# Kernel tuning notes

Hardware: AMD Instinct MI355X
Metric: run time of the kernel (lower is better)

## Reference

```python
import jax, jax.numpy as jnp
import numpy as np
import math

K = 20; M = 10; N = K * M; DEG = N - 1; AJR = 30; HID = 96
NH = 4; HD = HID + 2 + K; DM = NH * HD  # 472


def _graph():
    # complete graph: node i receives edges from all j != i (fixed in-degree DEG)
    idx = jnp.arange(N)
    j = jnp.arange(DEG)
    srcs = jnp.where(j[None, :] < idx[:, None], j[None, :], j[None, :] + 1)  # [N, DEG]
    grp = idx // M
    same = (grp[srcs] == grp[:, None]).astype(jnp.float32)  # e_type[:,1]
    return srcs, same


def _pe_table(max_step, dim):
    pos = np.arange(max_step)[:, None].astype(np.float32)
    div = np.exp(np.arange(0, dim, 2).astype(np.float32) * -(math.log(10000.0) / dim))
    pe = np.zeros((max_step, dim), np.float32)
    pe[:, 0::2] = np.sin(pos * div)
    pe[:, 1::2] = np.cos(pos * div)
    return jnp.asarray(pe)


def _gcn(h, x, label, w, d, srcs, same, p):
    (l0w, l0b, l1w, l1b, l2w, l2b, l3w, l3b, l4w, l4b, l5w, l5b) = p
    t0 = 1.0 - same
    h_src = h[srcs]                      # [N, DEG, HID] gather
    we = w[..., None]
    n1_v = (h_src * we * t0[..., None]).sum(1) / (w * t0).sum(1, keepdims=True)
    n2_v = (h_src * we * same[..., None]).sum(1) / (w * same).sum(1, keepdims=True)
    n1_e = jnp.sort(d * t0, axis=1)[:, ::-1][:, :AJR]      # top-AJR cross-group dists
    n2_e = jnp.sort(d * same, axis=1)[:, ::-1][:, :M - 1]  # top-(m-1) same-group dists
    return jax.nn.relu(x @ l0w + l0b + label @ l1w + l1b + n1_v @ l2w + l2b
                       + n2_v @ l3w + l3b + n1_e @ l4w + l4b + n2_e @ l5w + l5b)


def _forward(x, label, h0, w, d,
             l0_w, l0_b, l1_w, l1_b, l2_w, l2_b, l3_w, l3_b, l4_w, l4_b, l5_w, l5_b,
             mha_w0, mha_b0, mha_w1, mha_b1, mha_w3, mha_b3,
             v1_w, v1_b, v2_w, v2_b, gnn_step, max_step, remain_step):
    srcs, same = _graph()
    gcn_p = (l0_w, l0_b, l1_w, l1_b, l2_w, l2_b, l3_w, l3_b, l4_w, l4_b, l5_w, l5_b)
    h = h0
    for _ in range(gnn_step):
        h = _gcn(h, x, label, w, d, srcs, same, gcn_p)
    pe = _pe_table(max_step, HID)
    h_full = jnp.concatenate([h + pe[remain_step], x, label], axis=1)  # [N, HD]
    gc = h_full.T @ label / M                                          # [HD, K]
    kv = jnp.tile(h_full, (1, NH))                                     # [N, DM]
    kh = (kv @ mha_w0 + mha_b0).reshape(N, NH, HD).transpose(1, 0, 2)  # keys use linears[0]
    vh = (kv @ mha_w1 + mha_b1).reshape(N, NH, HD).transpose(1, 0, 2)  # values use linears[1]
    h_rep = jnp.repeat(h_full, N, axis=0)      # torch repeat(1,n).view(n*n, hd)
    h_tile = jnp.tile(h_full, (N, 1))          # torch repeat(n,1)
    la_rep = jnp.repeat(label, N, axis=0) @ gc.T
    la_tile = jnp.tile(label, (N, 1)) @ gc.T
    Q1 = jnp.concatenate([h_rep, h_tile, la_rep, la_tile], axis=1)  # [N*N, DM]
    Q2 = jnp.concatenate([h_tile, h_rep, la_tile, la_rep], axis=1)
    inv_sqrt_dk = 1.0 / jnp.sqrt(jnp.float32(HD))

    def attend(Q):
        q = (Q @ mha_w0 + mha_b0).reshape(-1, NH, HD)
        s = jnp.einsum('bhd,hkd->bhk', q, kh) * inv_sqrt_dk
        p = jax.nn.softmax(s, axis=-1)
        o = jnp.einsum('bhk,hkd->bhd', p, vh).reshape(-1, DM)
        return o @ mha_w3 + mha_b3

    S = attend(Q1) + attend(Q2)               # [N*N, DM]
    S_a_encoding = S[:, None, :]              # [N*N, 1, DM]
    Q_sa = (jax.nn.relu(S @ v1_w + v1_b) @ v2_w + v2_b).squeeze()  # [N*N]
    return S_a_encoding, h, h_full, Q_sa


def setup_inputs() -> dict:
    key = jax.random.key(0)
    ks = jax.random.split(key, 32)
    def rn(i, shape, s=1.0):
        return jax.random.normal(ks[i], shape, jnp.float32) * s
    grp = jnp.arange(N) // M
    label = jax.nn.one_hot(grp, K, dtype=jnp.float32)
    return {
        'x': rn(0, (N, 2)),
        'label': label,
        'h0': rn(1, (N, HID)),
        'w': jax.random.uniform(ks[2], (N, DEG), jnp.float32, 0.1, 1.0),
        'd': jax.random.uniform(ks[3], (N, DEG), jnp.float32, 0.0, 1.0),
        'l0_w': rn(4, (2, HID), 0.5), 'l0_b': rn(5, (HID,), 0.05),
        'l1_w': rn(6, (K, HID), 0.2), 'l1_b': rn(7, (HID,), 0.05),
        'l2_w': rn(8, (HID, HID), 0.1), 'l2_b': rn(9, (HID,), 0.05),
        'l3_w': rn(10, (HID, HID), 0.1), 'l3_b': rn(11, (HID,), 0.05),
        'l4_w': rn(12, (AJR, HID), 0.15), 'l4_b': rn(13, (HID,), 0.05),
        'l5_w': rn(14, (M - 1, HID), 0.3), 'l5_b': rn(15, (HID,), 0.05),
        'mha_w0': rn(16, (DM, DM), 0.04), 'mha_b0': rn(17, (DM,), 0.02),
        'mha_w1': rn(18, (DM, DM), 0.04), 'mha_b1': rn(19, (DM,), 0.02),
        'mha_w3': rn(20, (DM, DM), 0.04), 'mha_b3': rn(21, (DM,), 0.02),
        'v1_w': rn(22, (DM, HID // 2), 0.04), 'v1_b': rn(23, (HID // 2,), 0.02),
        'v2_w': rn(24, (HID // 2, 1), 0.1), 'v2_b': rn(25, (1,), 0.02),
        'gnn_step': 2, 'max_step': 50, 'remain_step': 10,
    }


def reference(x, label, h0, w, d,
              l0_w, l0_b, l1_w, l1_b, l2_w, l2_b, l3_w, l3_b, l4_w, l4_b, l5_w, l5_b,
              mha_w0, mha_b0, mha_w1, mha_b1, mha_w3, mha_b3,
              v1_w, v1_b, v2_w, v2_b, gnn_step, max_step, remain_step):
    return _forward(x, label, h0, w, d,
                    l0_w, l0_b, l1_w, l1_b, l2_w, l2_b, l3_w, l3_b, l4_w, l4_b, l5_w, l5_b,
                    mha_w0, mha_b0, mha_w1, mha_b1, mha_w3, mha_b3,
                    v1_w, v1_b, v2_w, v2_b, gnn_step, max_step, remain_step)
```

## Files before the change

kernel.cpp:

```cpp
#include <hip/hip_runtime.h>
#include <hip/hip_bf16.h>
#include <math.h>

typedef unsigned short ushort;
typedef unsigned int uint;

#define NV 200
#define DEG 199
#define HID 96
#define KG 20
#define MG 10
#define AJR 30
#define NH 4
#define HD 118
#define DM 472
#define NN 40000
#define NT 20100
#define NTP 20160

#define WS_BASE   0
#define WS_H1     19200
#define WS_H2     38400
#define WS_HFULL  57600
#define WS_KHF    194952
#define WS_VHF    289352
#define WS_B1     383752
#define WS_B2     478152
#define WS_SC1    572552
#define WS_SC2    732552
#define WS_ZT     1315464

#define OFF_H   18880000
#define OFF_HF  18899200
#define OFF_Q   18922800

typedef __attribute__((ext_vector_type(8))) short short8v;
typedef __attribute__((ext_vector_type(4))) float float4v;

__device__ __forceinline__ ushort f2bf(float f) {
  uint u = __float_as_uint(f);
  uint r = (u + 0x7fffu + ((u >> 16) & 1u)) >> 16;
  return (ushort)r;
}
__device__ __forceinline__ uint packbf(float a, float b) {
  __hip_bfloat162 h2 = __float22bfloat162_rn(make_float2(a, b));
  union { __hip_bfloat162 h; uint u; } c;
  c.h = h2;
  return c.u;
}

__device__ __forceinline__ int triOff(int i) {
  return i * 200 - ((i * (i - 1)) >> 1);
}
__device__ __forceinline__ void p2ij(int p, int& io, int& jo) {
  float s = sqrtf((float)(160801 - 8 * p));
  int i = (int)((401.0f - s) * 0.5f);
  if (i < 0) i = 0;
  if (i > 199) i = 199;
  while (i > 0 && triOff(i) > p) --i;
  while (i < 199 && triOff(i + 1) <= p) ++i;
  io = i;
  jo = i + (p - triOff(i));
}

__global__ __launch_bounds__(256) void k_base(
    const float* __restrict__ x, const float* __restrict__ dmat,
    const float* __restrict__ label,
    const float* __restrict__ l0w, const float* __restrict__ l0b,
    const float* __restrict__ l1w, const float* __restrict__ l1b,
    const float* __restrict__ l2b, const float* __restrict__ l3b,
    const float* __restrict__ l4w, const float* __restrict__ l4b,
    const float* __restrict__ l5w, const float* __restrict__ l5b,
    float* __restrict__ base) {
  int i = blockIdx.x; int t = threadIdx.x;
  int g = i / MG;
  __shared__ float sv[256];
  __shared__ float sn2[9];
  float v = -1.0f;
  if (t < DEG) {
    int u = (t < i) ? t : t + 1;
    if (u / MG != g) v = dmat[i * DEG + t];
  }
  sv[t] = v;
  __syncthreads();
  for (int k2 = 2; k2 <= 256; k2 <<= 1) {
    for (int jj = k2 >> 1; jj > 0; jj >>= 1) {
      int ixj = t ^ jj;
      if (ixj > t) {
        float a = sv[t], b = sv[ixj];
        bool sw = ((t & k2) == 0) ? (a < b) : (a > b);
        if (sw) { sv[t] = b; sv[ixj] = a; }
      }
      __syncthreads();
    }
  }
  if (t == 0) {
    float tmp[9];
    for (int q = 0; q < 9; q++) tmp[q] = dmat[i * DEG + MG * g + q];
    for (int a2 = 1; a2 < 9; a2++) {
      float key = tmp[a2]; int b2 = a2 - 1;
      while (b2 >= 0 && tmp[b2] < key) { tmp[b2 + 1] = tmp[b2]; b2--; }
      tmp[b2 + 1] = key;
    }
    for (int q = 0; q < 9; q++) sn2[q] = tmp[q];
  }
  __syncthreads();
  if (t < HID) {
    float acc = l0b[t] + l1b[t] + l2b[t] + l3b[t] + l4b[t] + l5b[t];
    acc += x[i * 2 + 0] * l0w[t] + x[i * 2 + 1] * l0w[HID + t];
    for (int k = 0; k < KG; k++) acc += label[i * KG + k] * l1w[k * HID + t];
    for (int q = 0; q < AJR; q++) acc += sv[q] * l4w[q * HID + t];
    for (int q = 0; q < 9; q++) acc += sn2[q] * l5w[q * HID + t];
    base[i * HID + t] = acc;
  }
}

__global__ __launch_bounds__(512) void k_gcn4(
    const float* __restrict__ hin, const float* __restrict__ base,
    const float* __restrict__ w, const float* __restrict__ l2w,
    const float* __restrict__ l3w, float* __restrict__ hout) {
  int i = blockIdx.x; int t = threadIdx.x;
  int g = i / MG;
  __shared__ float pJ[4][HID], wJ[4][HID];
  __shared__ float n1s[HID], n2s[HID];
  __shared__ float m[4][HID];
  if (t < 384) {
    int q = t / HID;
    int c = t - q * HID;
    int j0 = q * 50, j1 = (q == 3) ? DEG : (j0 + 50);
    float acc = 0.f, ws = 0.f;
    for (int j = j0; j < j1; j++) {
      int u = (j < i) ? j : j + 1;
      if (u / MG != g) {
        float wj = w[i * DEG + j];
        acc += wj * hin[u * HID + c];
        ws += wj;
      }
    }
    pJ[q][c] = acc; wJ[q][c] = ws;
  } else if (t < 416) {
#pragma unroll
    for (int q2 = 0; q2 < 3; q2++) {
      int dd = (t - 384) * 3 + q2;
      float acc = 0.f, ws = 0.f;
      for (int u = MG * g; u < MG * g + MG; u++) {
        if (u == i) continue;
        int j = (u < i) ? u : u - 1;
        float wj = w[i * DEG + j];
        acc += wj * hin[u * HID + dd];
        ws += wj;
      }
      n2s[dd] = acc / ws;
    }
  }
  __syncthreads();
  if (t < HID)
    n1s[t] = (pJ[0][t] + pJ[1][t] + pJ[2][t] + pJ[3][t]) /
             (wJ[0][t] + wJ[1][t] + wJ[2][t] + wJ[3][t]);
  __syncthreads();
  if (t < 384) {
    int q = t / HID, c = t - q * HID;
    int d0 = q * 24;
    float acc = 0.f;
    for (int dd = d0; dd < d0 + 24; dd++)
      acc += n1s[dd] * l2w[dd * HID + c] + n2s[dd] * l3w[dd * HID + c];
    m[q][c] = acc;
  }
  __syncthreads();
  if (t < HID)
    hout[i * HID + t] =
        fmaxf(base[i * HID + t] + m[0][t] + m[1][t] + m[2][t] + m[3][t], 0.f);
}

__global__ __launch_bounds__(128) void k_hfull(
    const float* __restrict__ h, const float* __restrict__ x,
    const float* __restrict__ label, const int* __restrict__ remain_step,
    float* __restrict__ hfull, float* __restrict__ out_h,
    float* __restrict__ out_hf) {
  int i = blockIdx.x; int t = threadIdx.x;
  if (t < HD) {
    float v;
    if (t < HID) {
      int p = *remain_step;
      int t2 = t & ~1;
      float div = expf(-(float)t2 * (logf(10000.f) / (float)HID));
      float ang = (float)p * div;
      float pe = (t & 1) ? cosf(ang) : sinf(ang);
      float hv = h[i * HID + t];
      out_h[i * HID + t] = hv;
      v = hv + pe;
    } else if (t < HID + 2) {
      v = x[i * 2 + (t - HID)];
    } else {
      v = label[i * KG + (t - HID - 2)];
    }
    hfull[i * HD + t] = v;
    out_hf[i * HD + t] = v;
  }
}

__global__ __launch_bounds__(256) void k_kvB(
    const float* __restrict__ hfull,
    const float* __restrict__ w0, const float* __restrict__ b0v,
    const float* __restrict__ w1, const float* __restrict__ b1v,
    float* __restrict__ khfT, float* __restrict__ vhf,
    float* __restrict__ B1, float* __restrict__ B2) {
  int i = blockIdx.x; int t = threadIdx.x; int g = i / MG;
  int half = blockIdx.y;
  __shared__ float hr[HD], gr[HD];
  if (t < HD) {
    hr[t] = hfull[i * HD + t];
    float s = 0.f;
    for (int q = 0; q < MG; q++) s += hfull[(g * MG + q) * HD + t];
    gr[t] = s * 0.1f;
  }
  __syncthreads();
  for (int c = half * 236 + t; c < 236 + half * 236; c += 256) {
    const float* w0c = w0 + c;
    const float* w1c = w1 + c;
    float d0 = 0.f, d1 = 0.f, d2 = 0.f, d3 = 0.f;
    float g2 = 0.f, g3 = 0.f;
    float e0 = 0.f, e1 = 0.f, e2 = 0.f, e3 = 0.f;
    for (int dd = 0; dd < HD; dd++) {
      float hv = hr[dd], gv = gr[dd];
      float a0 = w0c[dd * DM];
      float a1 = w0c[(HD + dd) * DM];
      float a2 = w0c[(2 * HD + dd) * DM];
      float a3 = w0c[(3 * HD + dd) * DM];
      d0 += hv * a0; d1 += hv * a1; d2 += hv * a2; d3 += hv * a3;
      g2 += gv * a2; g3 += gv * a3;
      e0 += hv * w1c[dd * DM];
      e1 += hv * w1c[(HD + dd) * DM];
      e2 += hv * w1c[(2 * HD + dd) * DM];
      e3 += hv * w1c[(3 * HD + dd) * DM];
    }
    float b0c = b0v[c];
    khfT[c * NV + i] = b0c + d0 + d1 + d2 + d3;
    vhf[i * DM + c] = b1v[c] + e0 + e1 + e2 + e3;
    B1[i * DM + c] = d0 + g2;
    B2[i * DM + c] = b0c + d1 + g3;
  }
}

__global__ __launch_bounds__(256) void k_SC(
    const float* __restrict__ B1, const float* __restrict__ B2,
    const float* __restrict__ khfT, float* __restrict__ SC1,
    float* __restrict__ SC2) {
  int i = blockIdx.x; int t = threadIdx.x;
  int qtr = blockIdx.y;
  const float scl = 1.4426950408889634f / sqrtf((float)HD);
  __shared__ float b1r[DM], b2r[DM];
  for (int c = t; c < DM; c += 256) { b1r[c] = B1[i * DM + c]; b2r[c] = B2[i * DM + c]; }
  __syncthreads();
  for (int p = qtr * 200 + t; p < qtr * 200 + 200; p += 256) {
    int h = p / NV, k = p - h * NV;
    float s1a = 0.f, s2a = 0.f;
    const float* kc = khfT + (size_t)h * HD * NV + k;
    const float* b1h = b1r + h * HD;
    const float* b2h = b2r + h * HD;
    for (int dd = 0; dd < HD; dd++) {
      float kv = kc[dd * NV];
      s1a += b1h[dd] * kv;
      s2a += b2h[dd] * kv;
    }
    SC1[h * NN + i * NV + k] = s1a * scl;
    SC2[h * NN + i * NV + k] = s2a * scl;
  }
}

__global__ __launch_bounds__(256) void k_ml(
    const float* __restrict__ SC1, const float* __restrict__ SC2,
    float* __restrict__ C) {
  int i = blockIdx.x;
  int h = blockIdx.y >> 1, jh = blockIdx.y & 1;
  int t = threadIdx.x;
  __shared__ float s1s[224];
  for (int k = t; k < 224; k += 256)
    s1s[k] = (k < NV) ? SC1[h * NN + i * NV + k] : -1e30f;
  __syncthreads();
  int l = t & 31;
  int g = t >> 5;
  const float* s2b = SC2 + h * NN;
  int it0 = jh ? 13 : 0, it1 = jh ? 25 : 13;
  for (int it = it0; it < it1; ++it) {
    int j = it * 8 + g;
    const float* row = s2b + j * NV;
    float v[7];
#pragma unroll
    for (int e = 0; e < 7; ++e) {
      int k = l + 32 * e;
      v[e] = (k < NV) ? (s1s[k] + row[k]) : -1e30f;
    }
    float m = v[0];
#pragma unroll
    for (int e = 1; e < 7; ++e) m = fmaxf(m, v[e]);
#pragma unroll
    for (int off = 16; off > 0; off >>= 1) m = fmaxf(m, __shfl_xor(m, off, 32));
    float s = 0.f;
#pragma unroll
    for (int e = 0; e < 7; ++e) s += exp2f(v[e] - m);
#pragma unroll
    for (int off = 16; off > 0; off >>= 1) s += __shfl_xor(s, off, 32);
    if (l == 0) C[h * NN + i * NV + j] = m + log2f(s);
  }
}

__global__ __launch_bounds__(256) void k_ZZT(
    const float* __restrict__ vhf, const float* __restrict__ w3,
    ushort* __restrict__ ZT) {
  int k = blockIdx.x, h = blockIdx.y;
  int t = threadIdx.x;
  __shared__ float vr[HD];
  if (k < NV && t < HD) vr[t] = vhf[k * DM + h * HD + t];
  __syncthreads();
  for (int c = t; c < 512; c += 256) {
    float a = 0.f;
    if (k < NV && c < DM) {
      for (int d = 0; d < HD; ++d) a += vr[d] * w3[(h * HD + d) * DM + c];
    }
    ZT[(size_t)c * 896 + h * 224 + k] = f2bf(a);
  }
}

__global__ __launch_bounds__(256) void k_sfusedT2(
    const float* __restrict__ SC1, const float* __restrict__ SC2,
    const float* __restrict__ C, const ushort* __restrict__ ZT,
    const float* __restrict__ b3, float* __restrict__ outS) {
  int t = threadIdx.x;
  int c0 = blockIdx.x * 128, p0 = blockIdx.y * 64;
  int lane = t & 63, wm = t >> 6;
  int frow = lane & 15, quad = lane >> 4;
  __shared__ __align__(16) ushort Bs[128 * 40];
  int p = p0 + wm * 16 + frow;
  bool bval = (p < NT);
  int iA = 0, jA = 0;
  if (bval) p2ij(p, iA, jA);
  int iN = iA * NV, jN = jA * NV;
  float4v acc[8];
#pragma unroll
  for (int n = 0; n < 8; ++n) acc[n] = (float4v)(0.f);
  int rB = t >> 1, khB = (t & 1) * 16;

  for (int h = 0; h < NH; ++h) {
    int hb = h * NN;
    const float* s1h = SC1 + hb;
    const float* s2h = SC2 + hb;
    float ci = bval ? C[hb + iN + jA] : 0.f;
    float cj = bval ? C[hb + jN + iA] : 0.f;
    for (int ks = 0; ks < 7; ++ks) {
      int kb = ks * 32 + quad * 8;
      bool kvalid = (kb + 7 < NV);
      union { uint4 q; short8v v; } af;
      if (bval && kvalid) {
        const float* q1i = s1h + iN + kb;
        const float* q2i = s2h + iN + kb;
        const float* q1j = s1h + jN + kb;
        const float* q2j = s2h + jN + kb;
        float4 a0 = *(const float4*)q1i,   a0b = *(const float4*)(q1i + 4);
        float4 b0 = *(const float4*)q2j,   b0b = *(const float4*)(q2j + 4);
        float4 d0 = *(const float4*)q1j,   d0b = *(const float4*)(q1j + 4);
        float4 e0 = *(const float4*)q2i,   e0b = *(const float4*)(q2i + 4);
        float p0_ = exp2f(a0.x + b0.x - ci) + exp2f(d0.x + e0.x - cj);
        float p1_ = exp2f(a0.y + b0.y - ci) + exp2f(d0.y + e0.y - cj);
        float p2_ = exp2f(a0.z + b0.z - ci) + exp2f(d0.z + e0.z - cj);
        float p3_ = exp2f(a0.w + b0.w - ci) + exp2f(d0.w + e0.w - cj);
        float p4_ = exp2f(a0b.x + b0b.x - ci) + exp2f(d0b.x + e0b.x - cj);
        float p5_ = exp2f(a0b.y + b0b.y - ci) + exp2f(d0b.y + e0b.y - cj);
        float p6_ = exp2f(a0b.z + b0b.z - ci) + exp2f(d0b.z + e0b.z - cj);
        float p7_ = exp2f(a0b.w + b0b.w - ci) + exp2f(d0b.w + e0b.w - cj);
        af.q.x = packbf(p0_, p1_);
        af.q.y = packbf(p2_, p3_);
        af.q.z = packbf(p4_, p5_);
        af.q.w = packbf(p6_, p7_);
      } else {
        af.q = make_uint4(0, 0, 0, 0);
      }
      const uint4* wp = (const uint4*)(ZT + (size_t)(c0 + rB) * 896 +
                                       h * 224 + ks * 32 + khB);
      uint4 bq0 = wp[0], bq1 = wp[1];
      __syncthreads();
      *(uint4*)&Bs[rB * 40 + khB] = bq0;
      *(uint4*)&Bs[rB * 40 + khB + 8] = bq1;
      __syncthreads();
#pragma unroll
      for (int n = 0; n < 8; ++n) {
        short8v bf = *(const short8v*)&Bs[(n * 16 + frow) * 40 + quad * 8];
        acc[n] = __builtin_amdgcn_mfma_f32_16x16x32_bf16(af.v, bf, acc[n],
                                                         0, 0, 0);
      }
    }
  }
  int ie[4], je[4];
#pragma unroll
  for (int r2 = 0; r2 < 4; ++r2) {
    int pe = p0 + wm * 16 + quad * 4 + r2;
    if (pe < NT) {
      p2ij(pe, ie[r2], je[r2]);
    } else {
      ie[r2] = -1; je[r2] = 0;
    }
  }
#pragma unroll
  for (int n = 0; n < 8; ++n) {
    int c = c0 + n * 16 + frow;
    if (c >= DM) continue;
    float bb = 2.0f * b3[c];
#pragma unroll
    for (int r2 = 0; r2 < 4; ++r2) {
      int ii = ie[r2];
      if (ii < 0) continue;
      int jj = je[r2];
      float v = acc[n][r2] + bb;
      outS[(size_t)(ii * NV + jj) * DM + c] = v;
      if (ii != jj) outS[(size_t)(jj * NV + ii) * DM + c] = v;
    }
  }
}

__global__ __launch_bounds__(256) void k_qsaT2(
    const float* __restrict__ S, const float* __restrict__ v1w,
    const float* __restrict__ v1b, const float* __restrict__ v2w,
    const float* __restrict__ v2b, float* __restrict__ outQ) {
  __shared__ float Ss[32][61];
  __shared__ float V1s[59][48];
  __shared__ float Ts[32][49];
  __shared__ int rowI[32], rowJ[32], rowOfs[32];
  int t = threadIdx.x;
  int p0b = blockIdx.x * 32;
  if (t < 32) {
    int p = p0b + t;
    if (p < NT) {
      int ii, jj; p2ij(p, ii, jj);
      rowI[t] = ii; rowJ[t] = jj; rowOfs[t] = ii * NV + jj;
    } else {
      rowI[t] = -1; rowJ[t] = 0; rowOfs[t] = 0;
    }
  }
  int ty2 = (t >> 4) * 2;
  int tx3 = (t & 15) * 3;
  float a00 = 0.f, a01 = 0.f, a02 = 0.f, a10 = 0.f, a11 = 0.f, a12 = 0.f;
  for (int k0 = 0; k0 < DM; k0 += 59) {
    __syncthreads();
    for (int e = t; e < 32 * 59; e += 256) {
      int r = e / 59, cc = e - r * 59;
      Ss[r][cc] = S[(size_t)rowOfs[r] * DM + k0 + cc];
    }
    for (int e = t; e < 59 * 48; e += 256) {
      int kk = e / 48, cc = e - kk * 48;
      V1s[kk][cc] = v1w[(size_t)(k0 + kk) * 48 + cc];
    }
    __syncthreads();
    for (int kk = 0; kk < 59; ++kk) {
      float s0 = Ss[ty2][kk], s1 = Ss[ty2 + 1][kk];
      float w0_ = V1s[kk][tx3], w1_ = V1s[kk][tx3 + 1], w2_ = V1s[kk][tx3 + 2];
      a00 += s0 * w0_; a01 += s0 * w1_; a02 += s0 * w2_;
      a10 += s1 * w0_; a11 += s1 * w1_; a12 += s1 * w2_;
    }
  }
  float b0 = v1b[tx3], b1 = v1b[tx3 + 1], b2 = v1b[tx3 + 2];
  Ts[ty2][tx3] = fmaxf(a00 + b0, 0.f);
  Ts[ty2][tx3 + 1] = fmaxf(a01 + b1, 0.f);
  Ts[ty2][tx3 + 2] = fmaxf(a02 + b2, 0.f);
  Ts[ty2 + 1][tx3] = fmaxf(a10 + b0, 0.f);
  Ts[ty2 + 1][tx3 + 1] = fmaxf(a11 + b1, 0.f);
  Ts[ty2 + 1][tx3 + 2] = fmaxf(a12 + b2, 0.f);
  __syncthreads();
  if (t < 32 && rowI[t] >= 0) {
    float q = v2b[0];
    for (int c = 0; c < 48; c++) q += Ts[t][c] * v2w[c];
    int ii = rowI[t], jj = rowJ[t];
    outQ[ii * NV + jj] = q;
    if (ii != jj) outQ[jj * NV + ii] = q;
  }
}

extern "C" void kernel_launch(void* const* d_in, const int* in_sizes, int n_in,
                              void* d_out, int out_size, void* d_ws,
                              size_t ws_size, hipStream_t stream) {
  const float* x = (const float*)d_in[0];
  const float* label = (const float*)d_in[1];
  const float* h0 = (const float*)d_in[2];
  const float* w = (const float*)d_in[3];
  const float* dmat = (const float*)d_in[4];
  const float* l0w = (const float*)d_in[5];
  const float* l0b = (const float*)d_in[6];
  const float* l1w = (const float*)d_in[7];
  const float* l1b = (const float*)d_in[8];
  const float* l2w = (const float*)d_in[9];
  const float* l2b = (const float*)d_in[10];
  const float* l3w = (const float*)d_in[11];
  const float* l3b = (const float*)d_in[12];
  const float* l4w = (const float*)d_in[13];
  const float* l4b = (const float*)d_in[14];
  const float* l5w = (const float*)d_in[15];
  const float* l5b = (const float*)d_in[16];
  const float* w0 = (const float*)d_in[17];
  const float* b0v = (const float*)d_in[18];
  const float* w1 = (const float*)d_in[19];
  const float* b1v = (const float*)d_in[20];
  const float* w3 = (const float*)d_in[21];
  const float* b3 = (const float*)d_in[22];
  const float* v1w = (const float*)d_in[23];
  const float* v1b = (const float*)d_in[24];
  const float* v2w = (const float*)d_in[25];
  const float* v2b = (const float*)d_in[26];
  const int* remain_step = (const int*)d_in[29];

  float* ws = (float*)d_ws;
  float* base = ws + WS_BASE;
  float* h1 = ws + WS_H1;
  float* h2 = ws + WS_H2;
  float* hfull = ws + WS_HFULL;
  float* khfT = ws + WS_KHF;
  float* vhf = ws + WS_VHF;
  float* B1 = ws + WS_B1;
  float* B2 = ws + WS_B2;
  float* SC1 = ws + WS_SC1;
  float* SC2 = ws + WS_SC2;
  ushort* ZT = (ushort*)(ws + WS_ZT);
  float* C = ws + WS_B1;

  float* outS = (float*)d_out;
  float* outH = outS + OFF_H;
  float* outHF = outS + OFF_HF;
  float* outQ = outS + OFF_Q;

  k_base<<<NV, 256, 0, stream>>>(x, dmat, label, l0w, l0b, l1w, l1b, l2b, l3b,
                                 l4w, l4b, l5w, l5b, base);
  k_gcn4<<<NV, 512, 0, stream>>>(h0, base, w, l2w, l3w, h1);
  k_gcn4<<<NV, 512, 0, stream>>>(h1, base, w, l2w, l3w, h2);
  k_hfull<<<NV, 128, 0, stream>>>(h2, x, label, remain_step, hfull, outH, outHF);
  k_kvB<<<dim3(NV, 2), 256, 0, stream>>>(hfull, w0, b0v, w1, b1v, khfT, vhf,
                                         B1, B2);
  k_ZZT<<<dim3(224, NH), 256, 0, stream>>>(vhf, w3, ZT);
  k_SC<<<dim3(NV, 4), 256, 0, stream>>>(B1, B2, khfT, SC1, SC2);
  k_ml<<<dim3(NV, NH * 2), 256, 0, stream>>>(SC1, SC2, C);
  k_sfusedT2<<<dim3(4, NTP / 64), 256, 0, stream>>>(SC1, SC2, C, ZT, b3, outS);
  k_qsaT2<<<(NT + 31) / 32, 256, 0, stream>>>(outS, v1w, v1b, v2w, v2b, outQ);
}
```

Baseline: 459.5 us.

## Fuse GCN prologue kernels and process two nodes per block in projections

Merges the base-term kernel with the first GCN step, and the second GCN step with the h_full construction, cutting the launch count from ten to eight. The K/V projection and the Z projection kernels now handle two nodes per block, so each weight load is shared by both nodes. The intent is to cut launch overhead and global weight traffic in the early stages. The cost is more registers per thread and fewer blocks, which lowers parallelism in the projection kernels.

After: 439.5 us. -4.4%, faster.

```diff
diff --git a/kernel.cpp b/kernel.cpp
--- a/kernel.cpp
+++ b/kernel.cpp
@@ -63,7 +63,7 @@
   jo = i + (p - triOff(i));
 }
 
-__global__ __launch_bounds__(256) void k_base(
+__global__ __launch_bounds__(512) void k_bgcn(
     const float* __restrict__ x, const float* __restrict__ dmat,
     const float* __restrict__ label,
     const float* __restrict__ l0w, const float* __restrict__ l0b,
@@ -71,25 +71,35 @@
     const float* __restrict__ l2b, const float* __restrict__ l3b,
     const float* __restrict__ l4w, const float* __restrict__ l4b,
     const float* __restrict__ l5w, const float* __restrict__ l5b,
-    float* __restrict__ base) {
+    const float* __restrict__ hin, const float* __restrict__ w,
+    const float* __restrict__ l2w, const float* __restrict__ l3w,
+    float* __restrict__ base, float* __restrict__ hout) {
   int i = blockIdx.x; int t = threadIdx.x;
   int g = i / MG;
   __shared__ float sv[256];
   __shared__ float sn2[9];
-  float v = -1.0f;
-  if (t < DEG) {
-    int u = (t < i) ? t : t + 1;
-    if (u / MG != g) v = dmat[i * DEG + t];
-  }
-  sv[t] = v;
+  __shared__ float bb[HID];
+  __shared__ float pJ[4][HID], wJ[4][HID];
+  __shared__ float n1s[HID], n2s[HID];
+  __shared__ float m[4][HID];
+  if (t < 256) {
+    float v = -1.0f;
+    if (t < DEG) {
+      int u = (t < i) ? t : t + 1;
+      if (u / MG != g) v = dmat[i * DEG + t];
+    }
+    sv[t] = v;
+  }
   __syncthreads();
   for (int k2 = 2; k2 <= 256; k2 <<= 1) {
     for (int jj = k2 >> 1; jj > 0; jj >>= 1) {
-      int ixj = t ^ jj;
-      if (ixj > t) {
-        float a = sv[t], b = sv[ixj];
-        bool sw = ((t & k2) == 0) ? (a < b) : (a > b);
-        if (sw) { sv[t] = b; sv[ixj] = a; }
+      if (t < 256) {
+        int ixj = t ^ jj;
+        if (ixj > t) {
+          float a = sv[t], b = sv[ixj];
+          bool sw = ((t & k2) == 0) ? (a < b) : (a > b);
+          if (sw) { sv[t] = b; sv[ixj] = a; }
+        }
       }
       __syncthreads();
     }
@@ -111,14 +121,64 @@
     for (int k = 0; k < KG; k++) acc += label[i * KG + k] * l1w[k * HID + t];
     for (int q = 0; q < AJR; q++) acc += sv[q] * l4w[q * HID + t];
     for (int q = 0; q < 9; q++) acc += sn2[q] * l5w[q * HID + t];
+    bb[t] = acc;
     base[i * HID + t] = acc;
   }
-}
-
-__global__ __launch_bounds__(512) void k_gcn4(
+  if (t < 384) {
+    int q = t / HID;
+    int c = t - q * HID;
+    int j0 = q * 50, j1 = (q == 3) ? DEG : (j0 + 50);
+    float acc = 0.f, ws = 0.f;
+    for (int j = j0; j < j1; j++) {
+      int u = (j < i) ? j : j + 1;
+      if (u / MG != g) {
+        float wj = w[i * DEG + j];
+        acc += wj * hin[u * HID + c];
+        ws += wj;
+      }
+    }
+    pJ[q][c] = acc; wJ[q][c] = ws;
+  } else if (t < 416) {
+#pragma unroll
+    for (int q2 = 0; q2 < 3; q2++) {
+      int dd = (t - 384) * 3 + q2;
+      float acc = 0.f, ws = 0.f;
+      for (int u = MG * g; u < MG * g + MG; u++) {
+        if (u == i) continue;
+        int j = (u < i) ? u : u - 1;
+        float wj = w[i * DEG + j];
+        acc += wj * hin[u * HID + dd];
+        ws += wj;
+      }
+      n2s[dd] = acc / ws;
+    }
+  }
+  __syncthreads();
+  if (t < HID)
+    n1s[t] = (pJ[0][t] + pJ[1][t] + pJ[2][t] + pJ[3][t]) /
+             (wJ[0][t] + wJ[1][t] + wJ[2][t] + wJ[3][t]);
+  __syncthreads();
+  if (t < 384) {
+    int q = t / HID, c = t - q * HID;
+    int d0 = q * 24;
+    float acc = 0.f;
+    for (int dd = d0; dd < d0 + 24; dd++)
+      acc += n1s[dd] * l2w[dd * HID + c] + n2s[dd] * l3w[dd * HID + c];
+    m[q][c] = acc;
+  }
+  __syncthreads();
+  if (t < HID)
+    hout[i * HID + t] =
+        fmaxf(bb[t] + m[0][t] + m[1][t] + m[2][t] + m[3][t], 0.f);
+}
+
+__global__ __launch_bounds__(512) void k_gcnhf(
     const float* __restrict__ hin, const float* __restrict__ base,
     const float* __restrict__ w, const float* __restrict__ l2w,
-    const float* __restrict__ l3w, float* __restrict__ hout) {
+    const float* __restrict__ l3w, const float* __restrict__ x,
+    const float* __restrict__ label, const int* __restrict__ remain_step,
+    float* __restrict__ hfull, float* __restrict__ out_h,
+    float* __restrict__ out_hf) {
   int i = blockIdx.x; int t = threadIdx.x;
   int g = i / MG;
   __shared__ float pJ[4][HID], wJ[4][HID];
@@ -167,78 +227,86 @@
     m[q][c] = acc;
   }
   __syncthreads();
-  if (t < HID)
-    hout[i * HID + t] =
+  if (t < HID) {
+    float hv =
         fmaxf(base[i * HID + t] + m[0][t] + m[1][t] + m[2][t] + m[3][t], 0.f);
-}
-
-__global__ __launch_bounds__(128) void k_hfull(
-    const float* __restrict__ h, const float* __restrict__ x,
-    const float* __restrict__ label, const int* __restrict__ remain_step,
-    float* __restrict__ hfull, float* __restrict__ out_h,
-    float* __restrict__ out_hf) {
-  int i = blockIdx.x; int t = threadIdx.x;
-  if (t < HD) {
-    float v;
-    if (t < HID) {
-      int p = *remain_step;
-      int t2 = t & ~1;
-      float div = expf(-(float)t2 * (logf(10000.f) / (float)HID));
-      float ang = (float)p * div;
-      float pe = (t & 1) ? cosf(ang) : sinf(ang);
-      float hv = h[i * HID + t];
-      out_h[i * HID + t] = hv;
-      v = hv + pe;
-    } else if (t < HID + 2) {
-      v = x[i * 2 + (t - HID)];
-    } else {
-      v = label[i * KG + (t - HID - 2)];
-    }
+    out_h[i * HID + t] = hv;
+    int p = *remain_step;
+    int t2 = t & ~1;
+    float div = expf(-(float)t2 * (logf(10000.f) / (float)HID));
+    float ang = (float)p * div;
+    float pe = (t & 1) ? cosf(ang) : sinf(ang);
+    float v = hv + pe;
     hfull[i * HD + t] = v;
     out_hf[i * HD + t] = v;
-  }
-}
-
-__global__ __launch_bounds__(256) void k_kvB(
+  } else if (t < HD) {
+    float v = (t < HID + 2) ? x[i * 2 + (t - HID)]
+                            : label[i * KG + (t - HID - 2)];
+    hfull[i * HD + t] = v;
+    out_hf[i * HD + t] = v;
+  }
+}
+
+__global__ __launch_bounds__(128) void k_kvB2(
     const float* __restrict__ hfull,
     const float* __restrict__ w0, const float* __restrict__ b0v,
     const float* __restrict__ w1, const float* __restrict__ b1v,
     float* __restrict__ khfT, float* __restrict__ vhf,
     float* __restrict__ B1, float* __restrict__ B2) {
-  int i = blockIdx.x; int t = threadIdx.x; int g = i / MG;
-  int half = blockIdx.y;
-  __shared__ float hr[HD], gr[HD];
+  int i0 = blockIdx.x, i1 = blockIdx.x + 100;
+  int q = blockIdx.y;
+  int t = threadIdx.x;
+  int g0 = i0 / MG, g1 = i1 / MG;
+  __shared__ float hr0[HD], gr0[HD], hr1[HD], gr1[HD];
   if (t < HD) {
-    hr[t] = hfull[i * HD + t];
-    float s = 0.f;
-    for (int q = 0; q < MG; q++) s += hfull[(g * MG + q) * HD + t];
-    gr[t] = s * 0.1f;
-  }
-  __syncthreads();
-  for (int c = half * 236 + t; c < 236 + half * 236; c += 256) {
+    hr0[t] = hfull[i0 * HD + t];
+    hr1[t] = hfull[i1 * HD + t];
+    float s0 = 0.f, s1 = 0.f;
+    for (int u = 0; u < MG; u++) {
+      s0 += hfull[(g0 * MG + u) * HD + t];
+      s1 += hfull[(g1 * MG + u) * HD + t];
+    }
+    gr0[t] = s0 * 0.1f;
+    gr1[t] = s1 * 0.1f;
+  }
+  __syncthreads();
+  int c = q * 118 + t;
+  if (t < 118) {
     const float* w0c = w0 + c;
     const float* w1c = w1 + c;
-    float d0 = 0.f, d1 = 0.f, d2 = 0.f, d3 = 0.f;
-    float g2 = 0.f, g3 = 0.f;
-    float e0 = 0.f, e1 = 0.f, e2 = 0.f, e3 = 0.f;
+    float d0a = 0.f, d1a = 0.f, d2a = 0.f, d3a = 0.f;
+    float g2a = 0.f, g3a = 0.f;
+    float e0a = 0.f, e1a = 0.f, e2a = 0.f, e3a = 0.f;
+    float d0b = 0.f, d1b = 0.f, d2b = 0.f, d3b = 0.f;
+    float g2b = 0.f, g3b = 0.f;
+    float e0b = 0.f, e1b = 0.f, e2b = 0.f, e3b = 0.f;
     for (int dd = 0; dd < HD; dd++) {
-      float hv = hr[dd], gv = gr[dd];
       float a0 = w0c[dd * DM];
       float a1 = w0c[(HD + dd) * DM];
       float a2 = w0c[(2 * HD + dd) * DM];
       float a3 = w0c[(3 * HD + dd) * DM];
-      d0 += hv * a0; d1 += hv * a1; d2 += hv * a2; d3 += hv * a3;
-      g2 += gv * a2; g3 += gv * a3;
-      e0 += hv * w1c[dd * DM];
-      e1 += hv * w1c[(HD + dd) * DM];
-      e2 += hv * w1c[(2 * HD + dd) * DM];
-      e3 += hv * w1c[(3 * HD + dd) * DM];
-    }
-    float b0c = b0v[c];
-    khfT[c * NV + i] = b0c + d0 + d1 + d2 + d3;
-    vhf[i * DM + c] = b1v[c] + e0 + e1 + e2 + e3;
-    B1[i * DM + c] = d0 + g2;
-    B2[i * DM + c] = b0c + d1 + g3;
+      float b0 = w1c[dd * DM];
+      float b1 = w1c[(HD + dd) * DM];
+      float b2 = w1c[(2 * HD + dd) * DM];
+      float b3 = w1c[(3 * HD + dd) * DM];
+      float h0v = hr0[dd], g0v = gr0[dd];
+      float h1v = hr1[dd], g1v = gr1[dd];
+      d0a += h0v * a0; d1a += h0v * a1; d2a += h0v * a2; d3a += h0v * a3;
+      g2a += g0v * a2; g3a += g0v * a3;
+      e0a += h0v * b0; e1a += h0v * b1; e2a += h0v * b2; e3a += h0v * b3;
+      d0b += h1v * a0; d1b += h1v * a1; d2b += h1v * a2; d3b += h1v * a3;
+      g2b += g1v * a2; g3b += g1v * a3;
+      e0b += h1v * b0; e1b += h1v * b1; e2b += h1v * b2; e3b += h1v * b3;
+    }
+    float b0c = b0v[c], b1c = b1v[c];
+    khfT[c * NV + i0] = b0c + d0a + d1a + d2a + d3a;
+    vhf[i0 * DM + c] = b1c + e0a + e1a + e2a + e3a;
+    B1[i0 * DM + c] = d0a + g2a;
+    B2[i0 * DM + c] = b0c + d1a + g3a;
+    khfT[c * NV + i1] = b0c + d0b + d1b + d2b + d3b;
+    vhf[i1 * DM + c] = b1c + e0b + e1b + e2b + e3b;
+    B1[i1 * DM + c] = d0b + g2b;
+    B2[i1 * DM + c] = b0c + d1b + g3b;
   }
 }
 
@@ -305,20 +373,30 @@
   }
 }
 
-__global__ __launch_bounds__(256) void k_ZZT(
+__global__ __launch_bounds__(256) void k_ZZT2(
     const float* __restrict__ vhf, const float* __restrict__ w3,
     ushort* __restrict__ ZT) {
-  int k = blockIdx.x, h = blockIdx.y;
+  int k0 = blockIdx.x * 2, h = blockIdx.y;
   int t = threadIdx.x;
-  __shared__ float vr[HD];
-  if (k < NV && t < HD) vr[t] = vhf[k * DM + h * HD + t];
+  bool v0 = (k0 < NV), v1 = (k0 + 1 < NV);
+  __shared__ float vr0[HD], vr1[HD];
+  if (t < HD) {
+    vr0[t] = v0 ? vhf[k0 * DM + h * HD + t] : 0.f;
+    vr1[t] = v1 ? vhf[(k0 + 1) * DM + h * HD + t] : 0.f;
+  }
   __syncthreads();
   for (int c = t; c < 512; c += 256) {
-    float a = 0.f;
-    if (k < NV && c < DM) {
-      for (int d = 0; d < HD; ++d) a += vr[d] * w3[(h * HD + d) * DM + c];
-    }
-    ZT[(size_t)c * 896 + h * 224 + k] = f2bf(a);
+    float a0 = 0.f, a1 = 0.f;
+    if (c < DM && v0) {
+      for (int d = 0; d < HD; ++d) {
+        float wv = w3[(h * HD + d) * DM + c];
+        a0 += vr0[d] * wv;
+        a1 += vr1[d] * wv;
+      }
+    }
+    ushort* zp = ZT + (size_t)c * 896 + h * 224 + k0;
+    zp[0] = f2bf(a0);
+    zp[1] = f2bf(v1 ? a1 : 0.f);
   }
 }
 
@@ -509,7 +587,6 @@
   float* ws = (float*)d_ws;
   float* base = ws + WS_BASE;
   float* h1 = ws + WS_H1;
-  float* h2 = ws + WS_H2;
   float* hfull = ws + WS_HFULL;
   float* khfT = ws + WS_KHF;
   float* vhf = ws + WS_VHF;
@@ -525,14 +602,13 @@
   float* outHF = outS + OFF_HF;
   float* outQ = outS + OFF_Q;
 
-  k_base<<<NV, 256, 0, stream>>>(x, dmat, label, l0w, l0b, l1w, l1b, l2b, l3b,
-                                 l4w, l4b, l5w, l5b, base);
-  k_gcn4<<<NV, 512, 0, stream>>>(h0, base, w, l2w, l3w, h1);
-  k_gcn4<<<NV, 512, 0, stream>>>(h1, base, w, l2w, l3w, h2);
-  k_hfull<<<NV, 128, 0, stream>>>(h2, x, label, remain_step, hfull, outH, outHF);
-  k_kvB<<<dim3(NV, 2), 256, 0, stream>>>(hfull, w0, b0v, w1, b1v, khfT, vhf,
-                                         B1, B2);
-  k_ZZT<<<dim3(224, NH), 256, 0, stream>>>(vhf, w3, ZT);
+  k_bgcn<<<NV, 512, 0, stream>>>(x, dmat, label, l0w, l0b, l1w, l1b, l2b, l3b,
+                                 l4w, l4b, l5w, l5b, h0, w, l2w, l3w, base, h1);
+  k_gcnhf<<<NV, 512, 0, stream>>>(h1, base, w, l2w, l3w, x, label, remain_step,
+                                  hfull, outH, outHF);
+  k_kvB2<<<dim3(100, 4), 128, 0, stream>>>(hfull, w0, b0v, w1, b1v, khfT, vhf,
+                                           B1, B2);
+  k_ZZT2<<<dim3(112, NH), 256, 0, stream>>>(vhf, w3, ZT);
   k_SC<<<dim3(NV, 4), 256, 0, stream>>>(B1, B2, khfT, SC1, SC2);
   k_ml<<<dim3(NV, NH * 2), 256, 0, stream>>>(SC1, SC2, C);
   k_sfusedT2<<<dim3(4, NTP / 64), 256, 0, stream>>>(SC1, SC2, C, ZT, b3, outS);
```
